# Kernel tuning notes

Hardware: AMD Instinct MI355X
Metric: run time of the kernel (lower is better)

The kernel has to match this reference:

```python
import jax, jax.numpy as jnp
import numpy as np

N_NODES = 50000
N_EDGES = 800000
IN_CH = 128
HID_CH = 128   # 2 * out_channels
OUT_CH = 64


def setup_inputs() -> dict:
    key = jax.random.key(0)
    k1, k2, k3, k4 = jax.random.split(key, 4)
    x = jax.random.normal(k1, (N_NODES, IN_CH), dtype=jnp.float32)
    edge_index = jax.random.randint(k2, (2, N_EDGES), 0, N_NODES, dtype=jnp.int64)
    # Glorot-ish scaled weights
    W1 = jax.random.normal(k3, (IN_CH, HID_CH), dtype=jnp.float32) * (1.0 / np.sqrt(IN_CH))
    b1 = jnp.zeros((HID_CH,), dtype=jnp.float32)
    W2 = jax.random.normal(k4, (HID_CH, OUT_CH), dtype=jnp.float32) * (1.0 / np.sqrt(HID_CH))
    b2 = jnp.zeros((OUT_CH,), dtype=jnp.float32)
    return {"x": x, "edge_index": edge_index, "W1": W1, "b1": b1, "W2": W2, "b2": b2}


def _gcn_conv(x, src, dst, W, b):
    # PyG GCNConv: add self-loops, symmetric deg^-1/2 normalization,
    # linear transform, scatter-add aggregation, bias.
    n = x.shape[0]
    loop = jnp.arange(n, dtype=src.dtype)
    s = jnp.concatenate([src, loop])
    d = jnp.concatenate([dst, loop])
    ones = jnp.ones(s.shape[0], dtype=x.dtype)
    deg = jax.ops.segment_sum(ones, d, num_segments=n)  # [N]
    dinv = jnp.where(deg > 0, deg ** -0.5, 0.0)
    norm = dinv[s] * dinv[d]                             # [E+N]
    xw = x @ W                                           # [N, F_out]
    msg = xw[s] * norm[:, None]                          # gather + scale
    agg = jax.ops.segment_sum(msg, d, num_segments=n)    # scatter-add
    return agg + b


def reference(x, edge_index, W1, b1, W2, b2):
    src, dst = edge_index[0], edge_index[1]
    h = jax.nn.relu(_gcn_conv(x, src, dst, W1, b1))
    out = jax.nn.relu(_gcn_conv(h, src, dst, W2, b2))
    return out
```

## Files before the change

### kernel.cpp

```cpp
#include <hip/hip_runtime.h>
#include <hip/hip_fp16.h>

using half8 = __attribute__((ext_vector_type(8))) _Float16;
using f32x4 = __attribute__((ext_vector_type(4))) float;

#define MAXB 256
#define ECAP 5376
#define EPB  3200


__global__ void prep(const float* __restrict__ W1, const float* __restrict__ W2,
                     _Float16* __restrict__ W1p, _Float16* __restrict__ W2p,
                     int* __restrict__ bktcnt) {
    int tid = threadIdx.x;
    if (blockIdx.x == 0) bktcnt[tid] = 0;
    int idx = blockIdx.x * 256 + tid;
    if (idx < 32 * 512) {
        int f = idx >> 9, rem = idx & 511, l = rem >> 3, j = rem & 7;
        int kt = f >> 3, nt = f & 7;
        W1p[idx] = (_Float16)W1[(kt * 32 + (l >> 4) * 8 + j) * 128 + nt * 16 + (l & 15)];
    } else if (idx < 32 * 512 + 16 * 512) {
        int i2 = idx - 32 * 512;
        int f = i2 >> 9, rem = i2 & 511, l = rem >> 3, j = rem & 7;
        int kt = f >> 2, nt = f & 3;
        W2p[i2] = (_Float16)W2[(kt * 32 + (l >> 4) * 8 + j) * 64 + nt * 16 + (l & 15)];
    }
}


__global__ __launch_bounds__(256) void bin_sort(const int* __restrict__ src,
                                                const int* __restrict__ dst,
                                                int* __restrict__ bktcnt,
                                                unsigned int* __restrict__ entries,
                                                int E, int N) {
    __shared__ unsigned int ebuf[EPB];
    __shared__ unsigned char bbuf[EPB];
    __shared__ int cntL[MAXB], fillL[MAXB], baseL[MAXB];
    int tid = threadIdx.x;
    cntL[tid] = 0;
    __syncthreads();

    int e0 = blockIdx.x * EPB;
    int e1 = min(e0 + EPB, E);
    int m = e1 - e0;

    for (int i = tid; i < m; i += 256) {
        int e = e0 + i;
        int s = src[e], d = dst[e];
        int b = 0;
        unsigned int entry = 0xFFFFFFFFu;
        if ((unsigned)s < (unsigned)N && (unsigned)d < (unsigned)N) {
            b = d >> 8;
            entry = (unsigned)s | ((unsigned)(d & 255) << 16);
            atomicAdd(&cntL[b], 1);
        }
        ebuf[i] = entry;
        bbuf[i] = (unsigned char)b;
    }
    __syncthreads();

    int c = cntL[tid];
    if (c > 0) baseL[tid] = atomicAdd(&bktcnt[tid], c);
    fillL[tid] = 0;
    __syncthreads();

    for (int i = tid; i < m; i += 256) {
        unsigned int entry = ebuf[i];
        if (entry == 0xFFFFFFFFu) continue;
        int b = bbuf[i];
        int pos = atomicAdd(&fillL[b], 1);
        int idx = baseL[b] + pos;
        if (idx < ECAP) entries[(size_t)b * ECAP + idx] = entry;
    }
}


__global__ __launch_bounds__(256) void build_csr(const unsigned int* __restrict__ entries,
                                                 const int* __restrict__ bktcnt,
                                                 int* __restrict__ rowp, int* __restrict__ cnt,
                                                 float* __restrict__ dinv,
                                                 unsigned short* __restrict__ col_src,
                                                 int N, int nbkt) {
    __shared__ int sb[256];
    __shared__ int cntL[256], offL[256], fillL[256];
    int b = blockIdx.x, tid = threadIdx.x;

    int bv = (tid < nbkt) ? min(bktcnt[tid], ECAP) : 0;
    sb[tid] = bv;
    cntL[tid] = 0;
    __syncthreads();
    for (int off = 1; off < 256; off <<= 1) {
        int t = (tid >= off) ? sb[tid - off] : 0;
        __syncthreads();
        sb[tid] += t;
        __syncthreads();
    }
    int tot = min(bktcnt[b], ECAP);
    int base = sb[b] - tot;

    const unsigned int* sp = entries + (size_t)b * ECAP;
    for (int i = tid; i < tot; i += 256) atomicAdd(&cntL[(sp[i] >> 16) & 255], 1);
    __syncthreads();

    int v = cntL[tid];
    offL[tid] = v;
    __syncthreads();
    for (int off = 1; off < 256; off <<= 1) {
        int t = (tid >= off) ? offL[tid - off] : 0;
        __syncthreads();
        offL[tid] += t;
        __syncthreads();
    }

    int ex = offL[tid] - v;
    int node = (b << 8) + tid;
    if (node < N) {
        rowp[node] = base + ex;
        cnt[node]  = v;
        dinv[node] = rsqrtf((float)(v + 1));
    }
    fillL[tid] = ex;
    __syncthreads();

    for (int i = tid; i < tot; i += 256) {
        unsigned int e = sp[i];
        int slot = atomicAdd(&fillL[(e >> 16) & 255], 1);
        col_src[base + slot] = (unsigned short)(e & 0xFFFFu);
    }
}


__global__ void xd_half(const float* __restrict__ x, const float* __restrict__ dinv,
                        __half2* __restrict__ xd2, int n32) {
    int idx = blockIdx.x * 256 + threadIdx.x;
    if (idx >= n32) return;
    int row = idx >> 5;
    float di = dinv[row];
    float4 xv = *(const float4*)&x[(size_t)idx * 4];
    uint2 o;
    __half2 h0 = __float22half2_rn(make_float2(di * xv.x, di * xv.y));
    __half2 h1 = __float22half2_rn(make_float2(di * xv.z, di * xv.w));
    __builtin_memcpy(&o.x, &h0, 4);
    __builtin_memcpy(&o.y, &h1, 4);
    *(uint2*)&xd2[(size_t)idx * 2] = o;
}


__global__ void agg_x128_h(const __half2* __restrict__ x2, const int* __restrict__ rowp,
                           const int* __restrict__ cnt, const unsigned short* __restrict__ col,
                           const float* __restrict__ dinv, __half2* __restrict__ out2, int n) {
    int node = blockIdx.x * 4 + (threadIdx.x >> 6);
    if (node >= n) return;
    int lane = threadIdx.x & 63;
    float2 self = __half22float2(x2[(size_t)node * 64 + lane]);
    float ax[8], ay[8];
    ax[0] = self.x; ay[0] = self.y;
#pragma unroll
    for (int j = 1; j < 8; ++j) { ax[j] = 0.f; ay[j] = 0.f; }
    int p = rowp[node];
    int deg = cnt[node];
    int k = 0;
    for (; k + 16 <= deg; k += 16) {
        float2 v[16];
#pragma unroll
        for (int j = 0; j < 16; ++j) v[j] = __half22float2(x2[(size_t)col[p + k + j] * 64 + lane]);
#pragma unroll
        for (int j = 0; j < 16; ++j) { ax[j & 7] += v[j].x; ay[j & 7] += v[j].y; }
    }
    if (k + 8 <= deg) {
        float2 v[8];
#pragma unroll
        for (int j = 0; j < 8; ++j) v[j] = __half22float2(x2[(size_t)col[p + k + j] * 64 + lane]);
#pragma unroll
        for (int j = 0; j < 8; ++j) { ax[j] += v[j].x; ay[j] += v[j].y; }
        k += 8;
    }
    if (k + 4 <= deg) {
        float2 v[4];
#pragma unroll
        for (int j = 0; j < 4; ++j) v[j] = __half22float2(x2[(size_t)col[p + k + j] * 64 + lane]);
#pragma unroll
        for (int j = 0; j < 4; ++j) { ax[j] += v[j].x; ay[j] += v[j].y; }
        k += 4;
    }
    for (; k < deg; ++k) {
        float2 v = __half22float2(x2[(size_t)col[p + k] * 64 + lane]);
        ax[0] += v.x; ay[0] += v.y;
    }
    float axs = ((ax[0] + ax[1]) + (ax[2] + ax[3])) + ((ax[4] + ax[5]) + (ax[6] + ax[7]));
    float ays = ((ay[0] + ay[1]) + (ay[2] + ay[3])) + ((ay[4] + ay[5]) + (ay[6] + ay[7]));
    float di = dinv[node];
    __half2 o = __float22half2_rn(make_float2(di * axs, di * ays));
    unsigned int ob;
    __builtin_memcpy(&ob, &o, 4);
    __builtin_nontemporal_store(ob, (unsigned int*)&out2[(size_t)node * 64 + lane]);
}


__global__ __launch_bounds__(256) void mlp_mfma(const _Float16* __restrict__ axh,
                                                const _Float16* __restrict__ W1p,
                                                const float* __restrict__ b1,
                                                const _Float16* __restrict__ W2p,
                                                const float* __restrict__ dinv,
                                                _Float16* __restrict__ yh, int M) {
    __shared__ _Float16 sh[4][16][136];
    int t = threadIdx.x;
    int w = t >> 6, l = t & 63;
    int rlo = l & 15, khi = l >> 4;
    int row0 = blockIdx.x * 64 + w * 16;

    half8 a[4];
    int arow = row0 + rlo;
    const half8* arp = (const half8*)(axh + (size_t)arow * 128 + khi * 8);
#pragma unroll
    for (int kt = 0; kt < 4; ++kt) {
        half8 v = {};
        if (arow < M) v = __builtin_nontemporal_load(arp + kt * 4);
        a[kt] = v;
    }

    f32x4 acc[8];
#pragma unroll
    for (int nt = 0; nt < 8; ++nt) acc[nt] = (f32x4){0.f, 0.f, 0.f, 0.f};
#pragma unroll
    for (int nt = 0; nt < 8; ++nt) {
#pragma unroll
        for (int kt = 0; kt < 4; ++kt) {
            half8 b = *(const half8*)&W1p[(size_t)((kt * 8 + nt) * 64 + l) * 8];
            acc[nt] = __builtin_amdgcn_mfma_f32_16x16x32_f16(a[kt], b, acc[nt], 0, 0, 0);
        }
    }

#pragma unroll
    for (int nt = 0; nt < 8; ++nt) {
        float bb = b1[nt * 16 + rlo];
#pragma unroll
        for (int r = 0; r < 4; ++r)
            sh[w][khi * 4 + r][nt * 16 + rlo] = (_Float16)fmaxf(acc[nt][r] + bb, 0.f);
    }
    __syncthreads();

    half8 a2[4];
#pragma unroll
    for (int kt = 0; kt < 4; ++kt)
        a2[kt] = *(const half8*)&sh[w][rlo][kt * 32 + khi * 8];

    f32x4 acc2[4];
#pragma unroll
    for (int nt = 0; nt < 4; ++nt) acc2[nt] = (f32x4){0.f, 0.f, 0.f, 0.f};
#pragma unroll
    for (int nt = 0; nt < 4; ++nt) {
#pragma unroll
        for (int kt = 0; kt < 4; ++kt) {
            half8 b = *(const half8*)&W2p[(size_t)((kt * 4 + nt) * 64 + l) * 8];
            acc2[nt] = __builtin_amdgcn_mfma_f32_16x16x32_f16(a2[kt], b, acc2[nt], 0, 0, 0);
        }
    }

#pragma unroll
    for (int r = 0; r < 4; ++r) {
        int row = row0 + khi * 4 + r;
        if (row < M) {
            float dn = dinv[row];
#pragma unroll
            for (int nt = 0; nt < 4; ++nt)
                yh[(size_t)row * 64 + nt * 16 + rlo] = (_Float16)(acc2[nt][r] * dn);
        }
    }
}


__global__ void agg_y64_h(const __half* __restrict__ y, const int* __restrict__ rowp,
                          const int* __restrict__ cnt, const unsigned short* __restrict__ col,
                          const float* __restrict__ dinv, const float* __restrict__ bias,
                          float* __restrict__ out, int n) {
    int node = blockIdx.x * 4 + (threadIdx.x >> 6);
    if (node >= n) return;
    int lane = threadIdx.x & 63;
    const __half* yc = y + lane;
    float a[8];
    a[0] = __half2float(yc[(size_t)node * 64]);
#pragma unroll
    for (int j = 1; j < 8; ++j) a[j] = 0.f;
    int p = rowp[node];
    int deg = cnt[node];
    int k = 0;
    for (; k + 16 <= deg; k += 16) {
        float v[16];
#pragma unroll
        for (int j = 0; j < 16; ++j) v[j] = __half2float(yc[(size_t)col[p + k + j] * 64]);
#pragma unroll
        for (int j = 0; j < 16; ++j) a[j & 7] += v[j];
    }
    if (k + 8 <= deg) {
        float v[8];
#pragma unroll
        for (int j = 0; j < 8; ++j) v[j] = __half2float(yc[(size_t)col[p + k + j] * 64]);
#pragma unroll
        for (int j = 0; j < 8; ++j) a[j] += v[j];
        k += 8;
    }
    if (k + 4 <= deg) {
        float v[4];
#pragma unroll
        for (int j = 0; j < 4; ++j) v[j] = __half2float(yc[(size_t)col[p + k + j] * 64]);
#pragma unroll
        for (int j = 0; j < 4; ++j) a[j] += v[j];
        k += 4;
    }
    for (; k < deg; ++k) a[0] += __half2float(yc[(size_t)col[p + k] * 64]);
    float as = ((a[0] + a[1]) + (a[2] + a[3])) + ((a[4] + a[5]) + (a[6] + a[7]));
    float o = fmaxf(bias[lane] + dinv[node] * as, 0.f);
    __builtin_nontemporal_store(o, &out[(size_t)node * 64 + lane]);
}


extern "C" void kernel_launch(void* const* d_in, const int* in_sizes, int n_in,
                              void* d_out, int out_size, void* d_ws, size_t ws_size,
                              hipStream_t stream) {
    const float* x  = (const float*)d_in[0];
    const int*   ei = (const int*)d_in[1];
    const float* W1 = (const float*)d_in[2];
    const float* b1 = (const float*)d_in[3];
    const float* W2 = (const float*)d_in[4];
    const float* b2 = (const float*)d_in[5];
    float* out = (float*)d_out;

    const int N = in_sizes[0] / 128;
    const int E = in_sizes[1] / 2;
    const int nbkt = (N + 255) >> 8;
    const int* src = ei;
    const int* dst = ei + E;

    char* ws = (char*)d_ws;
    size_t off = 0;
    auto alloc = [&](size_t bytes) {
        void* p = ws + off;
        off += (bytes + 255) & ~(size_t)255;
        return p;
    };
    int*            bktcnt  = (int*)           alloc((size_t)MAXB * 4);
    int*            rowp    = (int*)           alloc((size_t)N * 4);
    int*            cnt     = (int*)           alloc((size_t)N * 4);
    float*          dinv    = (float*)         alloc((size_t)N * 4);
    unsigned int*   entries = (unsigned int*)  alloc((size_t)nbkt * ECAP * 4);
    unsigned short* col_src = (unsigned short*)alloc((size_t)E * 2);
    __half2*        xdh     = (__half2*)       alloc((size_t)N * 128 * 2);
    __half2*        axh     = (__half2*)       alloc((size_t)N * 128 * 2);
    __half2*        yh      = (__half2*)       alloc((size_t)N * 64 * 2);
    _Float16*       W1p     = (_Float16*)      alloc((size_t)32 * 512 * 2);
    _Float16*       W2p     = (_Float16*)      alloc((size_t)16 * 512 * 2);

    const int binBlocks = (E + EPB - 1) / EPB;

    prep<<<96, 256, 0, stream>>>(W1, W2, W1p, W2p, bktcnt);
    bin_sort<<<binBlocks, 256, 0, stream>>>(src, dst, bktcnt, entries, E, N);
    build_csr<<<nbkt, 256, 0, stream>>>(entries, bktcnt, rowp, cnt, dinv, col_src, N, nbkt);
    xd_half<<<(N * 32 + 255) / 256, 256, 0, stream>>>(x, dinv, xdh, N * 32);

    agg_x128_h<<<(N + 3) / 4, 256, 0, stream>>>(xdh, rowp, cnt, col_src, dinv, axh, N);
    mlp_mfma<<<(N + 63) / 64, 256, 0, stream>>>((const _Float16*)axh, W1p, b1, W2p, dinv,
                                                (_Float16*)yh, N);
    agg_y64_h<<<(N + 3) / 4, 256, 0, stream>>>((const __half*)yh, rowp, cnt, col_src, dinv, b2, out, N);
}
```

Measured before the change: 115.5 us.

## Fuse x-to-half conversion into bin_sort launch and apply source dinv during aggregation

The separate xd_half kernel, which prescaled x by dinv, is removed. Extra blocks appended to the bin-sort launch now convert x to fp16 unscaled, so that conversion overlaps with edge binning instead of waiting for build_csr to produce dinv. To compensate, the first aggregation kernel gathers dinv[src] per neighbor and multiplies it in. This removes one launch and a serialized pass over x, but adds a scattered dinv gather and an extra multiply per edge in agg_x128_h.

```diff
diff --git a/kernel.cpp b/kernel.cpp
--- a/kernel.cpp
+++ b/kernel.cpp
@@ -7,6 +7,7 @@
 #define MAXB 256
 #define ECAP 5376
 #define EPB  3200
+#define XHB  192
 
 
 __global__ void prep(const float* __restrict__ W1, const float* __restrict__ W2,
@@ -28,15 +29,31 @@
 }
 
 
-__global__ __launch_bounds__(256) void bin_sort(const int* __restrict__ src,
-                                                const int* __restrict__ dst,
-                                                int* __restrict__ bktcnt,
-                                                unsigned int* __restrict__ entries,
-                                                int E, int N) {
+__global__ __launch_bounds__(256) void bin_xh(const int* __restrict__ src,
+                                              const int* __restrict__ dst,
+                                              int* __restrict__ bktcnt,
+                                              unsigned int* __restrict__ entries,
+                                              const float* __restrict__ x,
+                                              __half2* __restrict__ xh,
+                                              int E, int N, int binBlocks) {
+    int tid = threadIdx.x;
+    if ((int)blockIdx.x >= binBlocks) {
+        int n32 = N * 32;
+        for (int idx = ((int)blockIdx.x - binBlocks) * 256 + tid; idx < n32; idx += XHB * 256) {
+            float4 xv = *(const float4*)&x[(size_t)idx * 4];
+            uint2 o;
+            __half2 h0 = __float22half2_rn(make_float2(xv.x, xv.y));
+            __half2 h1 = __float22half2_rn(make_float2(xv.z, xv.w));
+            __builtin_memcpy(&o.x, &h0, 4);
+            __builtin_memcpy(&o.y, &h1, 4);
+            *(uint2*)&xh[(size_t)idx * 2] = o;
+        }
+        return;
+    }
+
     __shared__ unsigned int ebuf[EPB];
     __shared__ unsigned char bbuf[EPB];
     __shared__ int cntL[MAXB], fillL[MAXB], baseL[MAXB];
-    int tid = threadIdx.x;
     cntL[tid] = 0;
     __syncthreads();
 
@@ -130,66 +147,70 @@
 }
 
 
-__global__ void xd_half(const float* __restrict__ x, const float* __restrict__ dinv,
-                        __half2* __restrict__ xd2, int n32) {
-    int idx = blockIdx.x * 256 + threadIdx.x;
-    if (idx >= n32) return;
-    int row = idx >> 5;
-    float di = dinv[row];
-    float4 xv = *(const float4*)&x[(size_t)idx * 4];
-    uint2 o;
-    __half2 h0 = __float22half2_rn(make_float2(di * xv.x, di * xv.y));
-    __half2 h1 = __float22half2_rn(make_float2(di * xv.z, di * xv.w));
-    __builtin_memcpy(&o.x, &h0, 4);
-    __builtin_memcpy(&o.y, &h1, 4);
-    *(uint2*)&xd2[(size_t)idx * 2] = o;
-}
-
-
 __global__ void agg_x128_h(const __half2* __restrict__ x2, const int* __restrict__ rowp,
                            const int* __restrict__ cnt, const unsigned short* __restrict__ col,
                            const float* __restrict__ dinv, __half2* __restrict__ out2, int n) {
     int node = blockIdx.x * 4 + (threadIdx.x >> 6);
     if (node >= n) return;
     int lane = threadIdx.x & 63;
+    float di = dinv[node];
     float2 self = __half22float2(x2[(size_t)node * 64 + lane]);
     float ax[8], ay[8];
-    ax[0] = self.x; ay[0] = self.y;
+    ax[0] = di * self.x; ay[0] = di * self.y;
 #pragma unroll
     for (int j = 1; j < 8; ++j) { ax[j] = 0.f; ay[j] = 0.f; }
     int p = rowp[node];
     int deg = cnt[node];
     int k = 0;
     for (; k + 16 <= deg; k += 16) {
+        int s[16];
+#pragma unroll
+        for (int j = 0; j < 16; ++j) s[j] = col[p + k + j];
+        float ds[16];
+#pragma unroll
+        for (int j = 0; j < 16; ++j) ds[j] = dinv[s[j]];
         float2 v[16];
 #pragma unroll
-        for (int j = 0; j < 16; ++j) v[j] = __half22float2(x2[(size_t)col[p + k + j] * 64 + lane]);
-#pragma unroll
-        for (int j = 0; j < 16; ++j) { ax[j & 7] += v[j].x; ay[j & 7] += v[j].y; }
+        for (int j = 0; j < 16; ++j) v[j] = __half22float2(x2[(size_t)s[j] * 64 + lane]);
+#pragma unroll
+        for (int j = 0; j < 16; ++j) { ax[j & 7] += ds[j] * v[j].x; ay[j & 7] += ds[j] * v[j].y; }
     }
     if (k + 8 <= deg) {
+        int s[8];
+#pragma unroll
+        for (int j = 0; j < 8; ++j) s[j] = col[p + k + j];
+        float ds[8];
+#pragma unroll
+        for (int j = 0; j < 8; ++j) ds[j] = dinv[s[j]];
         float2 v[8];
 #pragma unroll
-        for (int j = 0; j < 8; ++j) v[j] = __half22float2(x2[(size_t)col[p + k + j] * 64 + lane]);
-#pragma unroll
-        for (int j = 0; j < 8; ++j) { ax[j] += v[j].x; ay[j] += v[j].y; }
+        for (int j = 0; j < 8; ++j) v[j] = __half22float2(x2[(size_t)s[j] * 64 + lane]);
+#pragma unroll
+        for (int j = 0; j < 8; ++j) { ax[j] += ds[j] * v[j].x; ay[j] += ds[j] * v[j].y; }
         k += 8;
     }
     if (k + 4 <= deg) {
+        int s[4];
+#pragma unroll
+        for (int j = 0; j < 4; ++j) s[j] = col[p + k + j];
+        float ds[4];
+#pragma unroll
+        for (int j = 0; j < 4; ++j) ds[j] = dinv[s[j]];
         float2 v[4];
 #pragma unroll
-        for (int j = 0; j < 4; ++j) v[j] = __half22float2(x2[(size_t)col[p + k + j] * 64 + lane]);
-#pragma unroll
-        for (int j = 0; j < 4; ++j) { ax[j] += v[j].x; ay[j] += v[j].y; }
+        for (int j = 0; j < 4; ++j) v[j] = __half22float2(x2[(size_t)s[j] * 64 + lane]);
+#pragma unroll
+        for (int j = 0; j < 4; ++j) { ax[j] += ds[j] * v[j].x; ay[j] += ds[j] * v[j].y; }
         k += 4;
     }
     for (; k < deg; ++k) {
-        float2 v = __half22float2(x2[(size_t)col[p + k] * 64 + lane]);
-        ax[0] += v.x; ay[0] += v.y;
+        int s = col[p + k];
+        float dsv = dinv[s];
+        float2 v = __half22float2(x2[(size_t)s * 64 + lane]);
+        ax[0] += dsv * v.x; ay[0] += dsv * v.y;
     }
     float axs = ((ax[0] + ax[1]) + (ax[2] + ax[3])) + ((ax[4] + ax[5]) + (ax[6] + ax[7]));
     float ays = ((ay[0] + ay[1]) + (ay[2] + ay[3])) + ((ay[4] + ay[5]) + (ay[6] + ay[7]));
-    float di = dinv[node];
     __half2 o = __float22half2_rn(make_float2(di * axs, di * ays));
     unsigned int ob;
     __builtin_memcpy(&ob, &o, 4);
@@ -345,7 +366,7 @@
     float*          dinv    = (float*)         alloc((size_t)N * 4);
     unsigned int*   entries = (unsigned int*)  alloc((size_t)nbkt * ECAP * 4);
     unsigned short* col_src = (unsigned short*)alloc((size_t)E * 2);
-    __half2*        xdh     = (__half2*)       alloc((size_t)N * 128 * 2);
+    __half2*        xh      = (__half2*)       alloc((size_t)N * 128 * 2);
     __half2*        axh     = (__half2*)       alloc((size_t)N * 128 * 2);
     __half2*        yh      = (__half2*)       alloc((size_t)N * 64 * 2);
     _Float16*       W1p     = (_Float16*)      alloc((size_t)32 * 512 * 2);
@@ -354,11 +375,9 @@
     const int binBlocks = (E + EPB - 1) / EPB;
 
     prep<<<96, 256, 0, stream>>>(W1, W2, W1p, W2p, bktcnt);
-    bin_sort<<<binBlocks, 256, 0, stream>>>(src, dst, bktcnt, entries, E, N);
+    bin_xh<<<binBlocks + XHB, 256, 0, stream>>>(src, dst, bktcnt, entries, x, xh, E, N, binBlocks);
     build_csr<<<nbkt, 256, 0, stream>>>(entries, bktcnt, rowp, cnt, dinv, col_src, N, nbkt);
-    xd_half<<<(N * 32 + 255) / 256, 256, 0, stream>>>(x, dinv, xdh, N * 32);
-
-    agg_x128_h<<<(N + 3) / 4, 256, 0, stream>>>(xdh, rowp, cnt, col_src, dinv, axh, N);
+    agg_x128_h<<<(N + 3) / 4, 256, 0, stream>>>(xh, rowp, cnt, col_src, dinv, axh, N);
     mlp_mfma<<<(N + 63) / 64, 256, 0, stream>>>((const _Float16*)axh, W1p, b1, W2p, dinv,
                                                 (_Float16*)yh, N);
     agg_y64_h<<<(N + 3) / 4, 256, 0, stream>>>((const __half*)yh, rowp, cnt, col_src, dinv, b2, out, N);
```

After: 115.7 us. Within noise of the previous version (+0.2%).
